# Performance work log

Measured on AMD Instinct MI355X. Metric: run time of the kernel, lower is better.

## Reference

```python
import jax, jax.numpy as jnp
import numpy as np

D_MODEL = 256
N_HEADS = 8
HEAD_DIM = D_MODEL // N_HEADS
EPS = 1e-6


def setup_inputs() -> dict:
    key = jax.random.key(0)
    ks = jax.random.split(key, 12)
    B, L, S = 8, 8192, 8192
    scale = 1.0 / np.sqrt(D_MODEL)
    inp = {
        "queries": jax.random.normal(ks[0], (B, L, D_MODEL), jnp.float32),
        "keys": jax.random.normal(ks[1], (B, S, D_MODEL), jnp.float32),
        "values": jax.random.normal(ks[2], (B, S, D_MODEL), jnp.float32),
        "query_masks": jnp.ones((B, L), jnp.float32),
        "key_masks": jnp.ones((B, S), jnp.float32),
        # nn.Linear params (torch layout: W [out,in], y = x @ W.T + b)
        "Wq": jax.random.normal(ks[3], (D_MODEL, D_MODEL), jnp.float32) * scale,
        "bq": jax.random.normal(ks[4], (D_MODEL,), jnp.float32) * scale,
        "Wk": jax.random.normal(ks[5], (D_MODEL, D_MODEL), jnp.float32) * scale,
        "bk": jax.random.normal(ks[6], (D_MODEL,), jnp.float32) * scale,
        "Wv": jax.random.normal(ks[7], (D_MODEL, D_MODEL), jnp.float32) * scale,
        "bv": jax.random.normal(ks[8], (D_MODEL,), jnp.float32) * scale,
        "Wm": jax.random.normal(ks[9], (D_MODEL, D_MODEL), jnp.float32) * scale,
        "bm": jax.random.normal(ks[10], (D_MODEL,), jnp.float32) * scale,
    }
    return inp


def _feature_map(x):
    return jax.nn.elu(x) + 1.0


def reference(queries, keys, values, query_masks, key_masks,
              Wq, bq, Wk, bk, Wv, bv, Wm, bm):
    B, L, D = queries.shape
    S = keys.shape[1]
    H, hd = N_HEADS, HEAD_DIM

    q = (queries @ Wq.T + bq).reshape(B, L, H, hd)
    k = (keys @ Wk.T + bk).reshape(B, S, H, hd)
    v = (values @ Wv.T + bv).reshape(B, S, H, hd)

    Q = _feature_map(q) * query_masks[:, :, None, None]
    K = _feature_map(k) * key_masks[:, :, None, None]
    v = v * key_masks[:, :, None, None]

    # KV: [B,H,hd_v(m),hd_k(d)]
    KV = jnp.einsum("nshd,nshm->nhmd", K, v)
    Z = 1.0 / (jnp.einsum("nlhd,nhd->nlh", Q, K.sum(axis=1)) + EPS)
    V = jnp.einsum("nlhd,nhmd,nlh->nlhm", Q, KV, Z)
    return V.reshape(B, L, D) @ Wm.T + bm
```

## Files before the change

### kernel.cpp

```cpp
#include <hip/hip_runtime.h>
#include <math.h>


#define B_ 8
#define S_ 8192
#define D_ 256
#define H_ 8
#define EPS_ 1e-6f

typedef short short8 __attribute__((ext_vector_type(8)));
typedef float f32x16 __attribute__((ext_vector_type(16)));
typedef float f32x4 __attribute__((ext_vector_type(4)));

#define LDSA_OFF 0
#define LDSB_OFF 32768
#define LDSM_OFF 65536
#define LDSBQ_OFF 65792
#define LDS_KA 65792
#define LDS_KB 66816

__device__ __forceinline__ unsigned short f2bf(float f) {
  union { float f; unsigned u; } v; v.f = f;
  return (unsigned short)((v.u + 0x7fffu + ((v.u >> 16) & 1u)) >> 16);
}

__device__ __forceinline__ void stage_tile(const float* __restrict__ src,
                                           char* __restrict__ ldsA, int tid) {
  const float4* s4 = (const float4*)src;
#pragma unroll
  for (int i = 0; i < 16; ++i) {
    float4 v = s4[i * 256 + tid];
    int f = i * 256 + tid;
    int tok = f >> 6, r = f & 63, g = r >> 1, j = r & 1;
    ushort4 h4 = make_ushort4(f2bf(v.x), f2bf(v.y), f2bf(v.z), f2bf(v.w));
    *(ushort4*)(ldsA + ((g * 64 + (tok ^ (g & 31))) * 16 + j * 8)) = h4;
  }
}

__global__ void kPrep(const float* __restrict__ Wq, const float* __restrict__ Wk,
                      const float* __restrict__ Wv, const float* __restrict__ Wm,
                      unsigned short* __restrict__ Wf) {
  int idx = blockIdx.x * 256 + threadIdx.x;
  int wsel = idx >> 13, g = (idx >> 8) & 31, o = idx & 255;
  const float* W = wsel == 0 ? Wq : wsel == 1 ? Wk : wsel == 2 ? Wv : Wm;
  const float* p = W + o * 256 + g * 8;
  ushort4 a = make_ushort4(f2bf(p[0]), f2bf(p[1]), f2bf(p[2]), f2bf(p[3]));
  ushort4 c = make_ushort4(f2bf(p[4]), f2bf(p[5]), f2bf(p[6]), f2bf(p[7]));
  *(ushort4*)(Wf + (size_t)idx * 8) = a;
  *(ushort4*)(Wf + (size_t)idx * 8 + 4) = c;
}

__global__ void __launch_bounds__(256, 2)
kA(const float* __restrict__ keys, const float* __restrict__ values,
   const float* __restrict__ kmask,
   const float* __restrict__ bk, const float* __restrict__ bv,
   const short8* __restrict__ WfK, const short8* __restrict__ WfV,
   float* __restrict__ kvpart, float* __restrict__ kspart,
   float* __restrict__ KV, float* __restrict__ Ksum, int use_atomic) {
  extern __shared__ char lds[];
  char* ldsA = lds + LDSA_OFF;
  char* ldsB = lds + LDSB_OFF;
  float* ldsM = (float*)(lds + LDSM_OFF);
  const int tid = threadIdx.x;
  const int w = tid >> 6, lane = tid & 63, lo = lane & 31, kg = lane >> 5;
  const int blk = blockIdx.x, b = blockIdx.y;

  const float bk0 = bk[w * 64 + lo], bk1 = bk[w * 64 + 32 + lo];
  const float bv0 = bv[w * 64 + lo], bv1 = bv[w * 64 + 32 + lo];

  f32x16 kvacc[2];
#pragma unroll
  for (int hh = 0; hh < 2; ++hh)
#pragma unroll
    for (int i = 0; i < 16; ++i) kvacc[hh][i] = 0.f;
  float ksacc0 = 0.f, ksacc1 = 0.f;

  for (int it = 0; it < 2; ++it) {
    const int t0 = (blk * 2 + it) * 64;
    __syncthreads();
    stage_tile(keys + ((size_t)b * S_ + t0) * D_, ldsA, tid);
    if (tid < 64) ldsM[tid] = kmask[(size_t)b * S_ + t0 + tid];
    __syncthreads();

    f32x16 acc[2][2];
#pragma unroll
    for (int mt = 0; mt < 2; ++mt)
#pragma unroll
      for (int nt = 0; nt < 2; ++nt)
#pragma unroll
        for (int i = 0; i < 16; ++i) acc[mt][nt][i] = 0.f;

#pragma unroll 2
    for (int ks = 0; ks < 16; ++ks) {
      const int g = 2 * ks + kg;
      short8 af[2], bf[2];
#pragma unroll
      for (int mt = 0; mt < 2; ++mt) {
        int tokb = mt * 32 + lo;
        af[mt] = *(const short8*)(ldsA + (g * 64 + (tokb ^ (g & 31))) * 16);
      }
#pragma unroll
      for (int nt = 0; nt < 2; ++nt) bf[nt] = WfK[g * 256 + w * 64 + nt * 32 + lo];
#pragma unroll
      for (int mt = 0; mt < 2; ++mt)
#pragma unroll
        for (int nt = 0; nt < 2; ++nt)
          acc[mt][nt] = __builtin_amdgcn_mfma_f32_32x32x16_bf16(af[mt], bf[nt],
                                                                acc[mt][nt], 0, 0, 0);
    }
    __syncthreads();

    stage_tile(values + ((size_t)b * S_ + t0) * D_, ldsA, tid);

#pragma unroll
    for (int mt = 0; mt < 2; ++mt)
#pragma unroll
      for (int nt = 0; nt < 2; ++nt) {
        const float bias = nt ? bk1 : bk0;
        const int o = w * 64 + nt * 32 + lo;
#pragma unroll
        for (int q = 0; q < 4; ++q) {
          float vv[4];
#pragma unroll
          for (int j2 = 0; j2 < 4; ++j2) {
            int r = 4 * q + j2;
            int tok = 8 * q + 4 * kg + 32 * mt + j2;
            float f = acc[mt][nt][r] + bias;
            f = f > 0.f ? f + 1.f : __expf(f);
            f *= ldsM[tok];
            if (nt == 0) ksacc0 += f; else ksacc1 += f;
            vv[j2] = f;
          }
          *(ushort4*)(ldsB + ((q + 4 * mt) * 256 + o) * 16 + kg * 8) =
              make_ushort4(f2bf(vv[0]), f2bf(vv[1]), f2bf(vv[2]), f2bf(vv[3]));
        }
      }
    __syncthreads();

#pragma unroll
    for (int mt = 0; mt < 2; ++mt)
#pragma unroll
      for (int nt = 0; nt < 2; ++nt)
#pragma unroll
        for (int i = 0; i < 16; ++i) acc[mt][nt][i] = 0.f;
#pragma unroll 2
    for (int ks = 0; ks < 16; ++ks) {
      const int g = 2 * ks + kg;
      short8 af[2], bf[2];
#pragma unroll
      for (int mt = 0; mt < 2; ++mt) {
        int tokb = mt * 32 + lo;
        af[mt] = *(const short8*)(ldsA + (g * 64 + (tokb ^ (g & 31))) * 16);
      }
#pragma unroll
      for (int nt = 0; nt < 2; ++nt) bf[nt] = WfV[g * 256 + w * 64 + nt * 32 + lo];
#pragma unroll
      for (int mt = 0; mt < 2; ++mt)
#pragma unroll
        for (int nt = 0; nt < 2; ++nt)
          acc[mt][nt] = __builtin_amdgcn_mfma_f32_32x32x16_bf16(af[mt], bf[nt],
                                                                acc[mt][nt], 0, 0, 0);
    }
    ushort4 vpk[2][2][4];
#pragma unroll
    for (int mt = 0; mt < 2; ++mt)
#pragma unroll
      for (int nt = 0; nt < 2; ++nt) {
        const float bias = nt ? bv1 : bv0;
#pragma unroll
        for (int q = 0; q < 4; ++q) {
          float vv[4];
#pragma unroll
          for (int j2 = 0; j2 < 4; ++j2) {
            int r = 4 * q + j2;
            int tok = 8 * q + 4 * kg + 32 * mt + j2;
            vv[j2] = (acc[mt][nt][r] + bias) * ldsM[tok];
          }
          vpk[mt][nt][q] = make_ushort4(f2bf(vv[0]), f2bf(vv[1]), f2bf(vv[2]), f2bf(vv[3]));
        }
      }
    __syncthreads();
#pragma unroll
    for (int mt = 0; mt < 2; ++mt)
#pragma unroll
      for (int nt = 0; nt < 2; ++nt) {
        const int o = w * 64 + nt * 32 + lo;
#pragma unroll
        for (int q = 0; q < 4; ++q)
          *(ushort4*)(ldsA + ((q + 4 * mt) * 256 + o) * 16 + kg * 8) = vpk[mt][nt][q];
      }

#pragma unroll
    for (int hh = 0; hh < 2; ++hh) {
      const int h = 2 * w + hh;
#pragma unroll
      for (int kv = 0; kv < 4; ++kv) {
        int tg = kv * 2 + kg;
        short8 akf = *(const short8*)(ldsB + (tg * 256 + h * 32 + lo) * 16);
        short8 bvf = *(const short8*)(ldsA + (tg * 256 + h * 32 + lo) * 16);
        kvacc[hh] = __builtin_amdgcn_mfma_f32_32x32x16_bf16(akf, bvf, kvacc[hh], 0, 0, 0);
      }
    }
  }

  float tot0 = ksacc0 + __shfl_xor(ksacc0, 32);
  float tot1 = ksacc1 + __shfl_xor(ksacc1, 32);
  if (use_atomic) {
    atomicAdd(&Ksum[b * 256 + w * 64 + (kg ? 32 : 0) + lo], kg ? tot1 : tot0);
#pragma unroll
    for (int hh = 0; hh < 2; ++hh) {
      int h = 2 * w + hh;
#pragma unroll
      for (int r = 0; r < 16; ++r) {
        int d = (r & 3) + 8 * (r >> 2) + 4 * kg;
        atomicAdd(&KV[(((size_t)b * H_ + h) * 32 + lo) * 32 + d], kvacc[hh][r]);
      }
    }
  } else {
    kspart[((size_t)b * 64 + blk) * 256 + w * 64 + (kg ? 32 : 0) + lo] = kg ? tot1 : tot0;
#pragma unroll
    for (int hh = 0; hh < 2; ++hh) {
      int h = 2 * w + hh;
      float* dst = kvpart + ((size_t)b * 64 + blk) * 8192 + ((h * 2 + kg) * 16) * 32 + lo;
#pragma unroll
      for (int r = 0; r < 16; ++r) dst[r * 32] = kvacc[hh][r];
    }
  }
}

__global__ void kR(const float* __restrict__ kvpart, const float* __restrict__ kspart,
                   float* __restrict__ KV, float* __restrict__ Ksum) {
  int idx = blockIdx.x * 256 + threadIdx.x;
  if (idx < 65536) {
    int b = idx >> 13, r2 = idx & 8191;
    int h = r2 >> 10, kg2 = (r2 >> 9) & 1, rr = (r2 >> 5) & 15, m = r2 & 31;
    const float* p = kvpart + (size_t)b * 64 * 8192 + r2;
    float s = 0.f;
#pragma unroll 8
    for (int j = 0; j < 64; ++j) s += p[(size_t)j * 8192];
    int d = (rr & 3) + 4 * kg2 + 8 * (rr >> 2);
    KV[(((size_t)b * H_ + h) * 32 + m) * 32 + d] = s;
  } else if (idx < 67584) {
    int t = idx - 65536;
    int b = t >> 8, o = t & 255;
    const float* p = kspart + (size_t)b * 64 * 256 + o;
    float s = 0.f;
#pragma unroll 8
    for (int j = 0; j < 64; ++j) s += p[j * 256];
    Ksum[t] = s;
  }
}

__global__ void __launch_bounds__(256, 2)
kB(const float* __restrict__ queries, const float* __restrict__ qmask,
   const float* __restrict__ bq, const float* __restrict__ bm,
   const short8* __restrict__ WfQ, const short8* __restrict__ WfM,
   const float* __restrict__ KV, const float* __restrict__ Ksum,
   float* __restrict__ out) {
  extern __shared__ char lds[];
  char* ldsA = lds + LDSA_OFF;
  char* ldsB = lds + LDSB_OFF;
  float* ldsM = (float*)(lds + LDSM_OFF);
  float* ldsBq = (float*)(lds + LDSBQ_OFF);
  const int tid = threadIdx.x;
  const int w = tid >> 6, lane = tid & 63, lo = lane & 31, kg = lane >> 5;
  const int blk = blockIdx.x, b = blockIdx.y;

  ldsBq[tid] = bq[tid];
  const float bm0 = bm[w * 64 + lo], bm1 = bm[w * 64 + 32 + lo];

  short8 kvf[2][2], ksf[2];
#pragma unroll
  for (int hh = 0; hh < 2; ++hh) {
    int h = 2 * w + hh;
#pragma unroll
    for (int ksd = 0; ksd < 2; ++ksd) {
      const float* p = KV + (((size_t)b * H_ + h) * 32 + lo) * 32 + ksd * 16 + kg * 8;
      short8 t;
#pragma unroll
      for (int j = 0; j < 8; ++j) t[j] = (short)f2bf(p[j]);
      kvf[hh][ksd] = t;
    }
    const float* ps = Ksum + b * 256 + h * 32 + (lane >> 4) * 8;
    short8 t2;
#pragma unroll
    for (int j = 0; j < 8; ++j) t2[j] = (short)f2bf(ps[j]);
    ksf[hh] = t2;
  }

  for (int it = 0; it < 2; ++it) {
    const int t0 = (blk * 2 + it) * 64;
    __syncthreads();
    stage_tile(queries + ((size_t)b * S_ + t0) * D_, ldsA, tid);
    if (tid < 64) ldsM[tid] = qmask[(size_t)b * S_ + t0 + tid];
    __syncthreads();

    f32x16 qa[2][2];
#pragma unroll
    for (int At = 0; At < 2; ++At)
#pragma unroll
      for (int Bt = 0; Bt < 2; ++Bt)
#pragma unroll
        for (int i = 0; i < 16; ++i) qa[At][Bt][i] = 0.f;
#pragma unroll 2
    for (int ks = 0; ks < 16; ++ks) {
      const int g = 2 * ks + kg;
      short8 aw[2], bx[2];
#pragma unroll
      for (int At = 0; At < 2; ++At) aw[At] = WfQ[g * 256 + w * 64 + At * 32 + lo];
#pragma unroll
      for (int Bt = 0; Bt < 2; ++Bt) {
        int tokb = Bt * 32 + lo;
        bx[Bt] = *(const short8*)(ldsA + (g * 64 + (tokb ^ (g & 31))) * 16);
      }
#pragma unroll
      for (int At = 0; At < 2; ++At)
#pragma unroll
        for (int Bt = 0; Bt < 2; ++Bt)
          qa[At][Bt] = __builtin_amdgcn_mfma_f32_32x32x16_bf16(aw[At], bx[Bt],
                                                               qa[At][Bt], 0, 0, 0);
    }
    __syncthreads();

#pragma unroll
    for (int At = 0; At < 2; ++At)
#pragma unroll
      for (int Bt = 0; Bt < 2; ++Bt) {
        int tok = Bt * 32 + lo;
        float qm = ldsM[tok];
#pragma unroll
        for (int q = 0; q < 4; ++q) {
          float vv[4];
#pragma unroll
          for (int j2 = 0; j2 < 4; ++j2) {
            int r = 4 * q + j2;
            int o = 8 * q + 4 * kg + 32 * At + 64 * w + j2;
            float f = qa[At][Bt][r] + ldsBq[o];
            f = f > 0.f ? f + 1.f : __expf(f);
            vv[j2] = f * qm;
          }
          *(ushort4*)(ldsB + ((q + 4 * At + 8 * w) * 64 + tok) * 16 + kg * 8) =
              make_ushort4(f2bf(vv[0]), f2bf(vv[1]), f2bf(vv[2]), f2bf(vv[3]));
        }
      }

    f32x16 pn[2][2];
    f32x4 pz[2][4];
#pragma unroll
    for (int hh = 0; hh < 2; ++hh) {
#pragma unroll
      for (int nt2 = 0; nt2 < 2; ++nt2)
#pragma unroll
        for (int i = 0; i < 16; ++i) pn[hh][nt2][i] = 0.f;
#pragma unroll
      for (int zt = 0; zt < 4; ++zt)
#pragma unroll
        for (int i = 0; i < 4; ++i) pz[hh][zt][i] = 0.f;
    }
#pragma unroll
    for (int hh = 0; hh < 2; ++hh) {
      int h = 2 * w + hh;
#pragma unroll
      for (int nt2 = 0; nt2 < 2; ++nt2)
#pragma unroll
        for (int ksd = 0; ksd < 2; ++ksd) {
          short8 bq8 = *(const short8*)(ldsB +
                        ((h * 4 + ksd * 2 + kg) * 64 + nt2 * 32 + lo) * 16);
          pn[hh][nt2] = __builtin_amdgcn_mfma_f32_32x32x16_bf16(kvf[hh][ksd], bq8,
                                                                pn[hh][nt2], 0, 0, 0);
        }
#pragma unroll
      for (int zt = 0; zt < 4; ++zt) {
        short8 bz = *(const short8*)(ldsB +
                      ((h * 4 + (lane >> 4)) * 64 + zt * 16 + (lane & 15)) * 16);
        pz[hh][zt] = __builtin_amdgcn_mfma_f32_16x16x32_bf16(ksf[hh], bz,
                                                             pz[hh][zt], 0, 0, 0);
      }
    }

#pragma unroll
    for (int hh = 0; hh < 2; ++hh) {
      int h = 2 * w + hh;
#pragma unroll
      for (int nt2 = 0; nt2 < 2; ++nt2) {
        int tok = nt2 * 32 + lo;
        float z = (lane & 16) ? pz[hh][nt2 * 2 + 1][0] : pz[hh][nt2 * 2][0];
        float inv = 1.0f / (z + EPS_);
#pragma unroll
        for (int q = 0; q < 4; ++q) {
          float vv[4];
#pragma unroll
          for (int j2 = 0; j2 < 4; ++j2) vv[j2] = pn[hh][nt2][4 * q + j2] * inv;
          *(ushort4*)(ldsA + ((h * 4 + q) * 64 + tok) * 16 + kg * 8) =
              make_ushort4(f2bf(vv[0]), f2bf(vv[1]), f2bf(vv[2]), f2bf(vv[3]));
        }
      }
    }
    __syncthreads();

    f32x16 oa[2][2];
#pragma unroll
    for (int mt = 0; mt < 2; ++mt)
#pragma unroll
      for (int nt2 = 0; nt2 < 2; ++nt2)
#pragma unroll
        for (int i = 0; i < 16; ++i) oa[mt][nt2][i] = 0.f;
#pragma unroll 2
    for (int ks = 0; ks < 16; ++ks) {
      const int g = 2 * ks + kg;
      short8 av[2], bw[2];
#pragma unroll
      for (int mt = 0; mt < 2; ++mt)
        av[mt] = *(const short8*)(ldsA + (g * 64 + mt * 32 + lo) * 16);
#pragma unroll
      for (int nt2 = 0; nt2 < 2; ++nt2) bw[nt2] = WfM[g * 256 + w * 64 + nt2 * 32 + lo];
#pragma unroll
      for (int mt = 0; mt < 2; ++mt)
#pragma unroll
        for (int nt2 = 0; nt2 < 2; ++nt2)
          oa[mt][nt2] = __builtin_amdgcn_mfma_f32_32x32x16_bf16(av[mt], bw[nt2],
                                                                oa[mt][nt2], 0, 0, 0);
    }
#pragma unroll
    for (int mt = 0; mt < 2; ++mt)
#pragma unroll
      for (int nt2 = 0; nt2 < 2; ++nt2) {
        const float bias = nt2 ? bm1 : bm0;
        const int o = w * 64 + nt2 * 32 + lo;
        float* dst = out + ((size_t)b * S_ + t0 + 32 * mt) * D_ + o;
#pragma unroll
        for (int r = 0; r < 16; ++r) {
          int tok = (r & 3) + 8 * (r >> 2) + 4 * kg;
          dst[(size_t)tok * D_] = oa[mt][nt2][r] + bias;
        }
      }
  }
}

extern "C" void kernel_launch(void* const* d_in, const int* in_sizes, int n_in,
                              void* d_out, int out_size, void* d_ws, size_t ws_size,
                              hipStream_t stream) {
  const float* queries = (const float*)d_in[0];
  const float* keys    = (const float*)d_in[1];
  const float* values  = (const float*)d_in[2];
  const float* qmask   = (const float*)d_in[3];
  const float* kmask   = (const float*)d_in[4];
  const float* Wq = (const float*)d_in[5];
  const float* bq = (const float*)d_in[6];
  const float* Wk = (const float*)d_in[7];
  const float* bk = (const float*)d_in[8];
  const float* Wv = (const float*)d_in[9];
  const float* bv = (const float*)d_in[10];
  const float* Wm = (const float*)d_in[11];
  const float* bm = (const float*)d_in[12];
  float* out = (float*)d_out;

  char* ws = (char*)d_ws;
  unsigned short* Wf = (unsigned short*)ws;
  float* KV   = (float*)(ws + 524288);
  float* Ksum = (float*)(ws + 786432);
  float* kvpart = (float*)(ws + 1048576);
  float* kspart = (float*)(ws + 1048576 + 16777216);
  const size_t need = 1048576 + 16777216 + 524288;
  const int use_atomic = (ws_size < need) ? 1 : 0;

  hipFuncSetAttribute(reinterpret_cast<const void*>(kA),
                      hipFuncAttributeMaxDynamicSharedMemorySize, LDS_KA);
  hipFuncSetAttribute(reinterpret_cast<const void*>(kB),
                      hipFuncAttributeMaxDynamicSharedMemorySize, LDS_KB);

  kPrep<<<128, 256, 0, stream>>>(Wq, Wk, Wv, Wm, Wf);
  if (use_atomic) hipMemsetAsync(ws + 524288, 0, 262144 + 8192, stream);

  const short8* Wf8 = (const short8*)Wf;
  kA<<<dim3(64, B_), 256, LDS_KA, stream>>>(keys, values, kmask, bk, bv,
      Wf8 + (size_t)1 * 8192, Wf8 + (size_t)2 * 8192, kvpart, kspart, KV, Ksum, use_atomic);
  if (!use_atomic) kR<<<264, 256, 0, stream>>>(kvpart, kspart, KV, Ksum);
  kB<<<dim3(64, B_), 256, LDS_KB, stream>>>(queries, qmask, bq, bm,
      Wf8, Wf8 + (size_t)3 * 8192, KV, Ksum, out);
}
```

Measured before the change: 306.6 us.

## Prefetch next tiles into registers and build MFMA fragments via lane shuffles

Both the K/V and Q kernels now issue the global loads for the next 64-token tile into registers while the current tile is being computed, so memory latency overlaps the MFMA work. Separate LDS buffers hold K and V. The projected K/V and Q feature maps are packed into MFMA operand fragments with cross-lane shuffles instead of a round trip through shared memory, which drops barriers. The normaliser Z becomes a scalar dot with Ksum held in LDS instead of an extra MFMA pass. The costs are much higher register pressure from the 16 to 32 float4 prefetch buffers, which could reduce occupancy, plus a slightly larger LDS footprint.

```diff
diff --git a/kernel.cpp b/kernel.cpp
--- a/kernel.cpp
+++ b/kernel.cpp
@@ -10,30 +10,109 @@
 
 typedef short short8 __attribute__((ext_vector_type(8)));
 typedef float f32x16 __attribute__((ext_vector_type(16)));
-typedef float f32x4 __attribute__((ext_vector_type(4)));
-
-#define LDSA_OFF 0
-#define LDSB_OFF 32768
-#define LDSM_OFF 65536
-#define LDSBQ_OFF 65792
-#define LDS_KA 65792
-#define LDS_KB 66816
-
-__device__ __forceinline__ unsigned short f2bf(float f) {
+
+#define KA_K 0
+#define KA_V 32768
+#define KA_M 65536
+#define KA_BYTES 66048
+#define KB_Q 0
+#define KB_O 32768
+#define KB_M 65536
+#define KB_S 66048
+#define KB_BQ 67072
+#define KB_BYTES 68096
+
+static __device__ __forceinline__ unsigned short f2bf(float f) {
   union { float f; unsigned u; } v; v.f = f;
   return (unsigned short)((v.u + 0x7fffu + ((v.u >> 16) & 1u)) >> 16);
 }
-
-__device__ __forceinline__ void stage_tile(const float* __restrict__ src,
-                                           char* __restrict__ ldsA, int tid) {
+static __device__ __forceinline__ unsigned pack2(float a, float b) {
+  return (unsigned)f2bf(a) | ((unsigned)f2bf(b) << 16);
+}
+
+static __device__ __forceinline__ void stage_issue(const float* __restrict__ src,
+                                                   int tid, float4* R) {
   const float4* s4 = (const float4*)src;
 #pragma unroll
+  for (int i = 0; i < 16; ++i) R[i] = s4[i * 256 + tid];
+}
+static __device__ __forceinline__ void stage_write(char* __restrict__ dst,
+                                                   int tid, const float4* R) {
+  const int w = tid >> 6, lane = tid & 63, g = lane >> 1, j = lane & 1;
+#pragma unroll
   for (int i = 0; i < 16; ++i) {
-    float4 v = s4[i * 256 + tid];
-    int f = i * 256 + tid;
-    int tok = f >> 6, r = f & 63, g = r >> 1, j = r & 1;
-    ushort4 h4 = make_ushort4(f2bf(v.x), f2bf(v.y), f2bf(v.z), f2bf(v.w));
-    *(ushort4*)(ldsA + ((g * 64 + (tok ^ (g & 31))) * 16 + j * 8)) = h4;
+    const int tok = 4 * i + w;
+    *(ushort4*)(dst + ((g * 64 + (tok ^ (g & 31))) * 16 + j * 8)) =
+        make_ushort4(f2bf(R[i].x), f2bf(R[i].y), f2bf(R[i].z), f2bf(R[i].w));
+  }
+}
+
+static __device__ __forceinline__ short8 mk_frag(unsigned w00, unsigned w01,
+                                                 unsigned w10, unsigned w11, int kg) {
+  unsigned a0 = kg ? w10 : w00, a1 = kg ? w11 : w01;
+  unsigned s0 = kg ? w00 : w10, s1 = kg ? w01 : w11;
+  unsigned r0 = __shfl_xor(s0, 32), r1 = __shfl_xor(s1, 32);
+  union { unsigned u[4]; short8 s8; } f;
+  f.u[0] = kg ? r0 : a0; f.u[1] = kg ? r1 : a1;
+  f.u[2] = kg ? a0 : r0; f.u[3] = kg ? a1 : r1;
+  return f.s8;
+}
+
+template <bool XOR>
+static __device__ __forceinline__ void gemm_std(const char* __restrict__ ldsX,
+                                                const short8* __restrict__ Wf,
+                                                int w, int lo, int kg, f32x16 acc[2][2]) {
+#pragma unroll
+  for (int a = 0; a < 2; ++a)
+#pragma unroll
+    for (int c = 0; c < 2; ++c)
+#pragma unroll
+      for (int i = 0; i < 16; ++i) acc[a][c][i] = 0.f;
+#pragma unroll 4
+  for (int ks = 0; ks < 16; ++ks) {
+    const int g = 2 * ks + kg;
+    short8 af[2], bf[2];
+#pragma unroll
+    for (int mt = 0; mt < 2; ++mt) {
+      int tok = mt * 32 + lo;
+      if (XOR) tok ^= (g & 31);
+      af[mt] = *(const short8*)(ldsX + (g * 64 + tok) * 16);
+    }
+#pragma unroll
+    for (int nt = 0; nt < 2; ++nt) bf[nt] = Wf[g * 256 + w * 64 + nt * 32 + lo];
+#pragma unroll
+    for (int mt = 0; mt < 2; ++mt)
+#pragma unroll
+      for (int nt = 0; nt < 2; ++nt)
+        acc[mt][nt] = __builtin_amdgcn_mfma_f32_32x32x16_bf16(af[mt], bf[nt],
+                                                              acc[mt][nt], 0, 0, 0);
+  }
+}
+
+static __device__ __forceinline__ void gemm_flip(const char* __restrict__ ldsX,
+                                                 const short8* __restrict__ Wf,
+                                                 int w, int lo, int kg, f32x16 acc[2][2]) {
+#pragma unroll
+  for (int a = 0; a < 2; ++a)
+#pragma unroll
+    for (int c = 0; c < 2; ++c)
+#pragma unroll
+      for (int i = 0; i < 16; ++i) acc[a][c][i] = 0.f;
+#pragma unroll 4
+  for (int ks = 0; ks < 16; ++ks) {
+    const int g = 2 * ks + kg;
+    short8 aw[2], bx[2];
+#pragma unroll
+    for (int At = 0; At < 2; ++At) aw[At] = Wf[g * 256 + w * 64 + At * 32 + lo];
+#pragma unroll
+    for (int Bt = 0; Bt < 2; ++Bt)
+      bx[Bt] = *(const short8*)(ldsX + (g * 64 + ((Bt * 32 + lo) ^ (g & 31))) * 16);
+#pragma unroll
+    for (int At = 0; At < 2; ++At)
+#pragma unroll
+      for (int Bt = 0; Bt < 2; ++Bt)
+        acc[At][Bt] = __builtin_amdgcn_mfma_f32_32x32x16_bf16(aw[At], bx[Bt],
+                                                              acc[At][Bt], 0, 0, 0);
   }
 }
 
@@ -44,10 +123,10 @@
   int wsel = idx >> 13, g = (idx >> 8) & 31, o = idx & 255;
   const float* W = wsel == 0 ? Wq : wsel == 1 ? Wk : wsel == 2 ? Wv : Wm;
   const float* p = W + o * 256 + g * 8;
-  ushort4 a = make_ushort4(f2bf(p[0]), f2bf(p[1]), f2bf(p[2]), f2bf(p[3]));
-  ushort4 c = make_ushort4(f2bf(p[4]), f2bf(p[5]), f2bf(p[6]), f2bf(p[7]));
-  *(ushort4*)(Wf + (size_t)idx * 8) = a;
-  *(ushort4*)(Wf + (size_t)idx * 8 + 4) = c;
+  *(ushort4*)(Wf + (size_t)idx * 8) =
+      make_ushort4(f2bf(p[0]), f2bf(p[1]), f2bf(p[2]), f2bf(p[3]));
+  *(ushort4*)(Wf + (size_t)idx * 8 + 4) =
+      make_ushort4(f2bf(p[4]), f2bf(p[5]), f2bf(p[6]), f2bf(p[7]));
 }
 
 __global__ void __launch_bounds__(256, 2)
@@ -58,12 +137,12 @@
    float* __restrict__ kvpart, float* __restrict__ kspart,
    float* __restrict__ KV, float* __restrict__ Ksum, int use_atomic) {
   extern __shared__ char lds[];
-  char* ldsA = lds + LDSA_OFF;
-  char* ldsB = lds + LDSB_OFF;
-  float* ldsM = (float*)(lds + LDSM_OFF);
-  const int tid = threadIdx.x;
-  const int w = tid >> 6, lane = tid & 63, lo = lane & 31, kg = lane >> 5;
+  char* ldsK = lds + KA_K;
+  char* ldsV = lds + KA_V;
+  float* ldsM = (float*)(lds + KA_M);
+  const int tid = threadIdx.x, w = tid >> 6, lane = tid & 63, lo = lane & 31, kg = lane >> 5;
   const int blk = blockIdx.x, b = blockIdx.y;
+  const size_t base = ((size_t)b * S_ + blk * 128) * D_;
 
   const float bk0 = bk[w * 64 + lo], bk1 = bk[w * 64 + 32 + lo];
   const float bv0 = bv[w * 64 + lo], bv1 = bv[w * 64 + 32 + lo];
@@ -73,95 +152,58 @@
   for (int hh = 0; hh < 2; ++hh)
 #pragma unroll
     for (int i = 0; i < 16; ++i) kvacc[hh][i] = 0.f;
-  float ksacc0 = 0.f, ksacc1 = 0.f;
-
+  float ks0 = 0.f, ks1 = 0.f;
+
+  float4 RK[16], RV[16];
+  stage_issue(keys + base, tid, RK);
+  stage_issue(values + base, tid, RV);
+  if (tid < 128) ldsM[tid] = kmask[(size_t)b * S_ + blk * 128 + tid];
+  stage_write(ldsK, tid, RK);
+
+#pragma unroll
   for (int it = 0; it < 2; ++it) {
-    const int t0 = (blk * 2 + it) * 64;
     __syncthreads();
-    stage_tile(keys + ((size_t)b * S_ + t0) * D_, ldsA, tid);
-    if (tid < 64) ldsM[tid] = kmask[(size_t)b * S_ + t0 + tid];
-    __syncthreads();
-
     f32x16 acc[2][2];
-#pragma unroll
-    for (int mt = 0; mt < 2; ++mt)
-#pragma unroll
-      for (int nt = 0; nt < 2; ++nt)
-#pragma unroll
-        for (int i = 0; i < 16; ++i) acc[mt][nt][i] = 0.f;
-
-#pragma unroll 2
-    for (int ks = 0; ks < 16; ++ks) {
-      const int g = 2 * ks + kg;
-      short8 af[2], bf[2];
-#pragma unroll
-      for (int mt = 0; mt < 2; ++mt) {
-        int tokb = mt * 32 + lo;
-        af[mt] = *(const short8*)(ldsA + (g * 64 + (tokb ^ (g & 31))) * 16);
-      }
-#pragma unroll
-      for (int nt = 0; nt < 2; ++nt) bf[nt] = WfK[g * 256 + w * 64 + nt * 32 + lo];
-#pragma unroll
-      for (int mt = 0; mt < 2; ++mt)
-#pragma unroll
-        for (int nt = 0; nt < 2; ++nt)
-          acc[mt][nt] = __builtin_amdgcn_mfma_f32_32x32x16_bf16(af[mt], bf[nt],
-                                                                acc[mt][nt], 0, 0, 0);
-    }
-    __syncthreads();
-
-    stage_tile(values + ((size_t)b * S_ + t0) * D_, ldsA, tid);
-
+    gemm_std<true>(ldsK, WfK, w, lo, kg, acc);
+
+    unsigned Wk_[2][2][4][2];
 #pragma unroll
     for (int mt = 0; mt < 2; ++mt)
 #pragma unroll
       for (int nt = 0; nt < 2; ++nt) {
         const float bias = nt ? bk1 : bk0;
-        const int o = w * 64 + nt * 32 + lo;
 #pragma unroll
         for (int q = 0; q < 4; ++q) {
           float vv[4];
 #pragma unroll
-          for (int j2 = 0; j2 < 4; ++j2) {
-            int r = 4 * q + j2;
-            int tok = 8 * q + 4 * kg + 32 * mt + j2;
-            float f = acc[mt][nt][r] + bias;
+          for (int c = 0; c < 4; ++c) {
+            const int tok = it * 64 + 32 * mt + 8 * q + 4 * kg + c;
+            float f = acc[mt][nt][4 * q + c] + bias;
             f = f > 0.f ? f + 1.f : __expf(f);
             f *= ldsM[tok];
-            if (nt == 0) ksacc0 += f; else ksacc1 += f;
-            vv[j2] = f;
+            if (nt == 0) ks0 += f; else ks1 += f;
+            vv[c] = f;
           }
-          *(ushort4*)(ldsB + ((q + 4 * mt) * 256 + o) * 16 + kg * 8) =
-              make_ushort4(f2bf(vv[0]), f2bf(vv[1]), f2bf(vv[2]), f2bf(vv[3]));
-        }
-      }
+          Wk_[mt][nt][q][0] = pack2(vv[0], vv[1]);
+          Wk_[mt][nt][q][1] = pack2(vv[2], vv[3]);
+        }
+      }
+    short8 kf[2][4];
+#pragma unroll
+    for (int nt = 0; nt < 2; ++nt)
+#pragma unroll
+      for (int mt = 0; mt < 2; ++mt)
+#pragma unroll
+        for (int sel = 0; sel < 2; ++sel)
+          kf[nt][2 * mt + sel] = mk_frag(Wk_[mt][nt][2 * sel][0], Wk_[mt][nt][2 * sel][1],
+                                         Wk_[mt][nt][2 * sel + 1][0], Wk_[mt][nt][2 * sel + 1][1], kg);
+
+    stage_write(ldsV, tid, RV);
+    if (it == 0) stage_issue(keys + base + 64 * D_, tid, RK);
     __syncthreads();
 
-#pragma unroll
-    for (int mt = 0; mt < 2; ++mt)
-#pragma unroll
-      for (int nt = 0; nt < 2; ++nt)
-#pragma unroll
-        for (int i = 0; i < 16; ++i) acc[mt][nt][i] = 0.f;
-#pragma unroll 2
-    for (int ks = 0; ks < 16; ++ks) {
-      const int g = 2 * ks + kg;
-      short8 af[2], bf[2];
-#pragma unroll
-      for (int mt = 0; mt < 2; ++mt) {
-        int tokb = mt * 32 + lo;
-        af[mt] = *(const short8*)(ldsA + (g * 64 + (tokb ^ (g & 31))) * 16);
-      }
-#pragma unroll
-      for (int nt = 0; nt < 2; ++nt) bf[nt] = WfV[g * 256 + w * 64 + nt * 32 + lo];
-#pragma unroll
-      for (int mt = 0; mt < 2; ++mt)
-#pragma unroll
-        for (int nt = 0; nt < 2; ++nt)
-          acc[mt][nt] = __builtin_amdgcn_mfma_f32_32x32x16_bf16(af[mt], bf[nt],
-                                                                acc[mt][nt], 0, 0, 0);
-    }
-    ushort4 vpk[2][2][4];
+    gemm_std<true>(ldsV, WfV, w, lo, kg, acc);
+    unsigned Wv_[2][2][4][2];
 #pragma unroll
     for (int mt = 0; mt < 2; ++mt)
 #pragma unroll
@@ -171,56 +213,52 @@
         for (int q = 0; q < 4; ++q) {
           float vv[4];
 #pragma unroll
-          for (int j2 = 0; j2 < 4; ++j2) {
-            int r = 4 * q + j2;
-            int tok = 8 * q + 4 * kg + 32 * mt + j2;
-            vv[j2] = (acc[mt][nt][r] + bias) * ldsM[tok];
+          for (int c = 0; c < 4; ++c) {
+            const int tok = it * 64 + 32 * mt + 8 * q + 4 * kg + c;
+            vv[c] = (acc[mt][nt][4 * q + c] + bias) * ldsM[tok];
           }
-          vpk[mt][nt][q] = make_ushort4(f2bf(vv[0]), f2bf(vv[1]), f2bf(vv[2]), f2bf(vv[3]));
-        }
-      }
-    __syncthreads();
-#pragma unroll
-    for (int mt = 0; mt < 2; ++mt)
-#pragma unroll
-      for (int nt = 0; nt < 2; ++nt) {
-        const int o = w * 64 + nt * 32 + lo;
-#pragma unroll
-        for (int q = 0; q < 4; ++q)
-          *(ushort4*)(ldsA + ((q + 4 * mt) * 256 + o) * 16 + kg * 8) = vpk[mt][nt][q];
-      }
-
+          Wv_[mt][nt][q][0] = pack2(vv[0], vv[1]);
+          Wv_[mt][nt][q][1] = pack2(vv[2], vv[3]);
+        }
+      }
+    short8 vf[2][4];
+#pragma unroll
+    for (int nt = 0; nt < 2; ++nt)
+#pragma unroll
+      for (int mt = 0; mt < 2; ++mt)
+#pragma unroll
+        for (int sel = 0; sel < 2; ++sel)
+          vf[nt][2 * mt + sel] = mk_frag(Wv_[mt][nt][2 * sel][0], Wv_[mt][nt][2 * sel][1],
+                                         Wv_[mt][nt][2 * sel + 1][0], Wv_[mt][nt][2 * sel + 1][1], kg);
+    if (it == 0) stage_issue(values + base + 64 * D_, tid, RV);
+
+#pragma unroll
+    for (int hh = 0; hh < 2; ++hh)
+#pragma unroll
+      for (int tg = 0; tg < 4; ++tg)
+        kvacc[hh] = __builtin_amdgcn_mfma_f32_32x32x16_bf16(kf[hh][tg], vf[hh][tg],
+                                                            kvacc[hh], 0, 0, 0);
+    if (it == 0) stage_write(ldsK, tid, RK);
+  }
+
+  const float tot0 = ks0 + __shfl_xor(ks0, 32);
+  const float tot1 = ks1 + __shfl_xor(ks1, 32);
+  if (use_atomic) {
+    atomicAdd(&Ksum[b * 256 + w * 64 + kg * 32 + lo], kg ? tot1 : tot0);
 #pragma unroll
     for (int hh = 0; hh < 2; ++hh) {
       const int h = 2 * w + hh;
 #pragma unroll
-      for (int kv = 0; kv < 4; ++kv) {
-        int tg = kv * 2 + kg;
-        short8 akf = *(const short8*)(ldsB + (tg * 256 + h * 32 + lo) * 16);
-        short8 bvf = *(const short8*)(ldsA + (tg * 256 + h * 32 + lo) * 16);
-        kvacc[hh] = __builtin_amdgcn_mfma_f32_32x32x16_bf16(akf, bvf, kvacc[hh], 0, 0, 0);
-      }
-    }
-  }
-
-  float tot0 = ksacc0 + __shfl_xor(ksacc0, 32);
-  float tot1 = ksacc1 + __shfl_xor(ksacc1, 32);
-  if (use_atomic) {
-    atomicAdd(&Ksum[b * 256 + w * 64 + (kg ? 32 : 0) + lo], kg ? tot1 : tot0);
+      for (int r = 0; r < 16; ++r) {
+        const int d = (r & 3) + 8 * (r >> 2) + 4 * kg;
+        atomicAdd(&KV[(((size_t)b * H_ + h) * 32 + lo) * 32 + d], kvacc[hh][r]);
+      }
+    }
+  } else {
+    kspart[((size_t)b * 64 + blk) * 256 + w * 64 + kg * 32 + lo] = kg ? tot1 : tot0;
 #pragma unroll
     for (int hh = 0; hh < 2; ++hh) {
-      int h = 2 * w + hh;
-#pragma unroll
-      for (int r = 0; r < 16; ++r) {
-        int d = (r & 3) + 8 * (r >> 2) + 4 * kg;
-        atomicAdd(&KV[(((size_t)b * H_ + h) * 32 + lo) * 32 + d], kvacc[hh][r]);
-      }
-    }
-  } else {
-    kspart[((size_t)b * 64 + blk) * 256 + w * 64 + (kg ? 32 : 0) + lo] = kg ? tot1 : tot0;
-#pragma unroll
-    for (int hh = 0; hh < 2; ++hh) {
-      int h = 2 * w + hh;
+      const int h = 2 * w + hh;
       float* dst = kvpart + ((size_t)b * 64 + blk) * 8192 + ((h * 2 + kg) * 16) * 32 + lo;
 #pragma unroll
       for (int r = 0; r < 16; ++r) dst[r * 32] = kvacc[hh][r];
@@ -258,180 +296,121 @@
    const float* __restrict__ KV, const float* __restrict__ Ksum,
    float* __restrict__ out) {
   extern __shared__ char lds[];
-  char* ldsA = lds + LDSA_OFF;
-  char* ldsB = lds + LDSB_OFF;
-  float* ldsM = (float*)(lds + LDSM_OFF);
-  float* ldsBq = (float*)(lds + LDSBQ_OFF);
-  const int tid = threadIdx.x;
-  const int w = tid >> 6, lane = tid & 63, lo = lane & 31, kg = lane >> 5;
+  char* ldsQ = lds + KB_Q;
+  char* ldsO = lds + KB_O;
+  float* ldsM = (float*)(lds + KB_M);
+  float* ldsS = (float*)(lds + KB_S);
+  float* ldsBq = (float*)(lds + KB_BQ);
+  const int tid = threadIdx.x, w = tid >> 6, lane = tid & 63, lo = lane & 31, kg = lane >> 5;
   const int blk = blockIdx.x, b = blockIdx.y;
-
+  const size_t base = ((size_t)b * S_ + blk * 128) * D_;
+
+  ldsS[tid] = Ksum[b * 256 + tid];
   ldsBq[tid] = bq[tid];
+  if (tid < 128) ldsM[tid] = qmask[(size_t)b * S_ + blk * 128 + tid];
   const float bm0 = bm[w * 64 + lo], bm1 = bm[w * 64 + 32 + lo];
 
-  short8 kvf[2][2], ksf[2];
-#pragma unroll
-  for (int hh = 0; hh < 2; ++hh) {
-    int h = 2 * w + hh;
+  short8 kvf[2][2];
+#pragma unroll
+  for (int hh = 0; hh < 2; ++hh)
 #pragma unroll
     for (int ksd = 0; ksd < 2; ++ksd) {
-      const float* p = KV + (((size_t)b * H_ + h) * 32 + lo) * 32 + ksd * 16 + kg * 8;
-      short8 t;
-#pragma unroll
-      for (int j = 0; j < 8; ++j) t[j] = (short)f2bf(p[j]);
-      kvf[hh][ksd] = t;
-    }
-    const float* ps = Ksum + b * 256 + h * 32 + (lane >> 4) * 8;
-    short8 t2;
-#pragma unroll
-    for (int j = 0; j < 8; ++j) t2[j] = (short)f2bf(ps[j]);
-    ksf[hh] = t2;
-  }
-
+      const float* p = KV + (((size_t)b * H_ + 2 * w + hh) * 32 + lo) * 32 + ksd * 16 + kg * 8;
+      float4 x0 = *(const float4*)p, x1 = *(const float4*)(p + 4);
+      union { unsigned u[4]; short8 s8; } t;
+      t.u[0] = pack2(x0.x, x0.y); t.u[1] = pack2(x0.z, x0.w);
+      t.u[2] = pack2(x1.x, x1.y); t.u[3] = pack2(x1.z, x1.w);
+      kvf[hh][ksd] = t.s8;
+    }
+
+  float4 RQ[16];
+  stage_issue(queries + base, tid, RQ);
+  stage_write(ldsQ, tid, RQ);
+
+#pragma unroll
   for (int it = 0; it < 2; ++it) {
-    const int t0 = (blk * 2 + it) * 64;
     __syncthreads();
-    stage_tile(queries + ((size_t)b * S_ + t0) * D_, ldsA, tid);
-    if (tid < 64) ldsM[tid] = qmask[(size_t)b * S_ + t0 + tid];
-    __syncthreads();
-
     f32x16 qa[2][2];
-#pragma unroll
-    for (int At = 0; At < 2; ++At)
-#pragma unroll
-      for (int Bt = 0; Bt < 2; ++Bt)
-#pragma unroll
-        for (int i = 0; i < 16; ++i) qa[At][Bt][i] = 0.f;
-#pragma unroll 2
-    for (int ks = 0; ks < 16; ++ks) {
-      const int g = 2 * ks + kg;
-      short8 aw[2], bx[2];
-#pragma unroll
-      for (int At = 0; At < 2; ++At) aw[At] = WfQ[g * 256 + w * 64 + At * 32 + lo];
+    gemm_flip(ldsQ, WfQ, w, lo, kg, qa);
+    if (it == 0) stage_issue(queries + base + 64 * D_, tid, RQ);
+
+    unsigned Wq_[2][2][4][2];
+    float inv_[2][2];
+#pragma unroll
+    for (int At = 0; At < 2; ++At) {
+      float kss[4][4], bql[4][4];
+#pragma unroll
+      for (int q = 0; q < 4; ++q)
+#pragma unroll
+        for (int c = 0; c < 4; ++c) {
+          const int o = w * 64 + At * 32 + 8 * q + 4 * kg + c;
+          kss[q][c] = ldsS[o];
+          bql[q][c] = ldsBq[o];
+        }
 #pragma unroll
       for (int Bt = 0; Bt < 2; ++Bt) {
-        int tokb = Bt * 32 + lo;
-        bx[Bt] = *(const short8*)(ldsA + (g * 64 + (tokb ^ (g & 31))) * 16);
-      }
-#pragma unroll
-      for (int At = 0; At < 2; ++At)
-#pragma unroll
-        for (int Bt = 0; Bt < 2; ++Bt)
-          qa[At][Bt] = __builtin_amdgcn_mfma_f32_32x32x16_bf16(aw[At], bx[Bt],
-                                                               qa[At][Bt], 0, 0, 0);
-    }
-    __syncthreads();
-
-#pragma unroll
-    for (int At = 0; At < 2; ++At)
-#pragma unroll
-      for (int Bt = 0; Bt < 2; ++Bt) {
-        int tok = Bt * 32 + lo;
-        float qm = ldsM[tok];
+        const float qm = ldsM[it * 64 + Bt * 32 + lo];
+        float z = 0.f;
 #pragma unroll
         for (int q = 0; q < 4; ++q) {
           float vv[4];
 #pragma unroll
-          for (int j2 = 0; j2 < 4; ++j2) {
-            int r = 4 * q + j2;
-            int o = 8 * q + 4 * kg + 32 * At + 64 * w + j2;
-            float f = qa[At][Bt][r] + ldsBq[o];
+          for (int c = 0; c < 4; ++c) {
+            float f = qa[At][Bt][4 * q + c] + bql[q][c];
             f = f > 0.f ? f + 1.f : __expf(f);
-            vv[j2] = f * qm;
+            f *= qm;
+            z += f * kss[q][c];
+            vv[c] = f;
           }
-          *(ushort4*)(ldsB + ((q + 4 * At + 8 * w) * 64 + tok) * 16 + kg * 8) =
-              make_ushort4(f2bf(vv[0]), f2bf(vv[1]), f2bf(vv[2]), f2bf(vv[3]));
-        }
-      }
-
-    f32x16 pn[2][2];
-    f32x4 pz[2][4];
+          Wq_[At][Bt][q][0] = pack2(vv[0], vv[1]);
+          Wq_[At][Bt][q][1] = pack2(vv[2], vv[3]);
+        }
+        const float zf = z + __shfl_xor(z, 32);
+        inv_[At][Bt] = 1.0f / (zf + EPS_);
+      }
+    }
+
 #pragma unroll
     for (int hh = 0; hh < 2; ++hh) {
-#pragma unroll
-      for (int nt2 = 0; nt2 < 2; ++nt2)
-#pragma unroll
-        for (int i = 0; i < 16; ++i) pn[hh][nt2][i] = 0.f;
-#pragma unroll
-      for (int zt = 0; zt < 4; ++zt)
-#pragma unroll
-        for (int i = 0; i < 4; ++i) pz[hh][zt][i] = 0.f;
-    }
-#pragma unroll
-    for (int hh = 0; hh < 2; ++hh) {
-      int h = 2 * w + hh;
-#pragma unroll
-      for (int nt2 = 0; nt2 < 2; ++nt2)
+      const int h = 2 * w + hh;
+#pragma unroll
+      for (int Bt = 0; Bt < 2; ++Bt) {
+        f32x16 pn;
+#pragma unroll
+        for (int i = 0; i < 16; ++i) pn[i] = 0.f;
 #pragma unroll
         for (int ksd = 0; ksd < 2; ++ksd) {
-          short8 bq8 = *(const short8*)(ldsB +
-                        ((h * 4 + ksd * 2 + kg) * 64 + nt2 * 32 + lo) * 16);
-          pn[hh][nt2] = __builtin_amdgcn_mfma_f32_32x32x16_bf16(kvf[hh][ksd], bq8,
-                                                                pn[hh][nt2], 0, 0, 0);
-        }
-#pragma unroll
-      for (int zt = 0; zt < 4; ++zt) {
-        short8 bz = *(const short8*)(ldsB +
-                      ((h * 4 + (lane >> 4)) * 64 + zt * 16 + (lane & 15)) * 16);
-        pz[hh][zt] = __builtin_amdgcn_mfma_f32_16x16x32_bf16(ksf[hh], bz,
-                                                             pz[hh][zt], 0, 0, 0);
-      }
-    }
-
-#pragma unroll
-    for (int hh = 0; hh < 2; ++hh) {
-      int h = 2 * w + hh;
-#pragma unroll
-      for (int nt2 = 0; nt2 < 2; ++nt2) {
-        int tok = nt2 * 32 + lo;
-        float z = (lane & 16) ? pz[hh][nt2 * 2 + 1][0] : pz[hh][nt2 * 2][0];
-        float inv = 1.0f / (z + EPS_);
-#pragma unroll
-        for (int q = 0; q < 4; ++q) {
-          float vv[4];
-#pragma unroll
-          for (int j2 = 0; j2 < 4; ++j2) vv[j2] = pn[hh][nt2][4 * q + j2] * inv;
-          *(ushort4*)(ldsA + ((h * 4 + q) * 64 + tok) * 16 + kg * 8) =
-              make_ushort4(f2bf(vv[0]), f2bf(vv[1]), f2bf(vv[2]), f2bf(vv[3]));
-        }
+          short8 qf = mk_frag(Wq_[hh][Bt][2 * ksd][0], Wq_[hh][Bt][2 * ksd][1],
+                              Wq_[hh][Bt][2 * ksd + 1][0], Wq_[hh][Bt][2 * ksd + 1][1], kg);
+          pn = __builtin_amdgcn_mfma_f32_32x32x16_bf16(kvf[hh][ksd], qf, pn, 0, 0, 0);
+        }
+        const float inv = inv_[hh][Bt];
+        const int tok = Bt * 32 + lo;
+#pragma unroll
+        for (int q = 0; q < 4; ++q)
+          *(ushort4*)(ldsO + ((h * 4 + q) * 64 + tok) * 16 + kg * 8) =
+              make_ushort4(f2bf(pn[4 * q + 0] * inv), f2bf(pn[4 * q + 1] * inv),
+                           f2bf(pn[4 * q + 2] * inv), f2bf(pn[4 * q + 3] * inv));
       }
     }
     __syncthreads();
 
     f32x16 oa[2][2];
+    gemm_std<false>(ldsO, WfM, w, lo, kg, oa);
+    if (it == 0) stage_write(ldsQ, tid, RQ);
+
+    const int t0 = blk * 128 + it * 64;
 #pragma unroll
     for (int mt = 0; mt < 2; ++mt)
 #pragma unroll
-      for (int nt2 = 0; nt2 < 2; ++nt2)
-#pragma unroll
-        for (int i = 0; i < 16; ++i) oa[mt][nt2][i] = 0.f;
-#pragma unroll 2
-    for (int ks = 0; ks < 16; ++ks) {
-      const int g = 2 * ks + kg;
-      short8 av[2], bw[2];
-#pragma unroll
-      for (int mt = 0; mt < 2; ++mt)
-        av[mt] = *(const short8*)(ldsA + (g * 64 + mt * 32 + lo) * 16);
-#pragma unroll
-      for (int nt2 = 0; nt2 < 2; ++nt2) bw[nt2] = WfM[g * 256 + w * 64 + nt2 * 32 + lo];
-#pragma unroll
-      for (int mt = 0; mt < 2; ++mt)
-#pragma unroll
-        for (int nt2 = 0; nt2 < 2; ++nt2)
-          oa[mt][nt2] = __builtin_amdgcn_mfma_f32_32x32x16_bf16(av[mt], bw[nt2],
-                                                                oa[mt][nt2], 0, 0, 0);
-    }
-#pragma unroll
-    for (int mt = 0; mt < 2; ++mt)
-#pragma unroll
-      for (int nt2 = 0; nt2 < 2; ++nt2) {
-        const float bias = nt2 ? bm1 : bm0;
-        const int o = w * 64 + nt2 * 32 + lo;
+      for (int nt = 0; nt < 2; ++nt) {
+        const float bias = nt ? bm1 : bm0;
+        const int o = w * 64 + nt * 32 + lo;
         float* dst = out + ((size_t)b * S_ + t0 + 32 * mt) * D_ + o;
 #pragma unroll
         for (int r = 0; r < 16; ++r) {
-          int tok = (r & 3) + 8 * (r >> 2) + 4 * kg;
-          dst[(size_t)tok * D_] = oa[mt][nt2][r] + bias;
+          const int tok = (r & 3) + 8 * (r >> 2) + 4 * kg;
+          dst[(size_t)tok * D_] = oa[mt][nt][r] + bias;
         }
       }
   }
@@ -465,17 +444,17 @@
   const int use_atomic = (ws_size < need) ? 1 : 0;
 
   hipFuncSetAttribute(reinterpret_cast<const void*>(kA),
-                      hipFuncAttributeMaxDynamicSharedMemorySize, LDS_KA);
+                      hipFuncAttributeMaxDynamicSharedMemorySize, KA_BYTES);
   hipFuncSetAttribute(reinterpret_cast<const void*>(kB),
-                      hipFuncAttributeMaxDynamicSharedMemorySize, LDS_KB);
+                      hipFuncAttributeMaxDynamicSharedMemorySize, KB_BYTES);
 
   kPrep<<<128, 256, 0, stream>>>(Wq, Wk, Wv, Wm, Wf);
   if (use_atomic) hipMemsetAsync(ws + 524288, 0, 262144 + 8192, stream);
 
   const short8* Wf8 = (const short8*)Wf;
-  kA<<<dim3(64, B_), 256, LDS_KA, stream>>>(keys, values, kmask, bk, bv,
+  kA<<<dim3(64, B_), 256, KA_BYTES, stream>>>(keys, values, kmask, bk, bv,
       Wf8 + (size_t)1 * 8192, Wf8 + (size_t)2 * 8192, kvpart, kspart, KV, Ksum, use_atomic);
   if (!use_atomic) kR<<<264, 256, 0, stream>>>(kvpart, kspart, KV, Ksum);
-  kB<<<dim3(64, B_), 256, LDS_KB, stream>>>(queries, qmask, bq, bm,
+  kB<<<dim3(64, B_), 256, KB_BYTES, stream>>>(queries, qmask, bq, bm,
       Wf8, Wf8 + (size_t)3 * 8192, KV, Ksum, out);
 }
```

Result: slower. 316.8 us (+3.3%).
